# Performance work log

Hardware: AMD Instinct MI355X
Metric: run time of the kernel (lower is better)

Reference implementation:

```python
import jax, jax.numpy as jnp
import numpy as np

B, IN_F, OUT_F, K = 8192, 1024, 4096, 2
S = 64  # sqrt(OUT_F)


def setup_inputs() -> dict:
    key = jax.random.key(0)
    k1, k2, k3, k4 = jax.random.split(key, 4)
    x = jax.random.normal(k1, (B, IN_F), dtype=jnp.float32)
    y = jax.random.normal(k2, (B, OUT_F), dtype=jnp.float32)
    weight = jax.random.normal(k3, (OUT_F, IN_F), dtype=jnp.float32) * (1.0 / np.sqrt(IN_F))
    bias = jax.random.normal(k4, (OUT_F,), dtype=jnp.float32) * (1.0 / np.sqrt(IN_F))
    return {"x": x, "y": y, "weight": weight, "bias": bias}


def reference(x, y, weight, bias):
    # fused GEMM + bias + residual add epilogue
    out_lin = jnp.einsum('bk,nk->bn', x, weight) + bias + y  # (B, OUT_F)
    feat = out_lin.reshape(B, S, S)
    # AvgPool2d(kernel=K, stride=K)
    s_out = S // K
    pooled = feat.reshape(B, s_out, K, s_out, K).mean(axis=(2, 4))  # (B, s_out, s_out)
    # divide by global mean of the pooled map
    mean_val = pooled.mean()
    normed = pooled / mean_val
    return normed[:, None, :, :]  # (B, 1, s_out, s_out)
```

## Files before the change

### kernel.cpp

```cpp
#include <hip/hip_runtime.h>
#include <stdint.h>


#define KDIM 1024
#define NP   1024
#define BM 128
#define BN 128
#define BK 64

typedef __bf16 bf16x8 __attribute__((ext_vector_type(8)));
typedef float f32x4 __attribute__((ext_vector_type(4)));
typedef _Float16 f16x4 __attribute__((ext_vector_type(4)));

__device__ __forceinline__ unsigned f2bf(float f) {
  union { float f; unsigned u; } v; v.f = f;
  unsigned r = v.u + 0x7fffu + ((v.u >> 16) & 1u);
  return r >> 16;
}

__device__ __forceinline__ void gload_lds16(const void* g, void* l) {
  __builtin_amdgcn_global_load_lds(
      (const __attribute__((address_space(1))) void*)g,
      (__attribute__((address_space(3))) void*)l, 16, 0, 0);
}

__global__ void k_prep(const float* __restrict__ x, const float* __restrict__ W,
                       const float* __restrict__ bias,
                       unsigned short* __restrict__ xb, unsigned short* __restrict__ wp,
                       float* __restrict__ biasp) {
  int b = blockIdx.x;
  int t = threadIdx.x;
  if (b < 4096) {
    int i = b * 256 + t;
    const float4* x4 = (const float4*)x;
    float4 a = x4[i * 2], c = x4[i * 2 + 1];
    uint4 o;
    o.x = f2bf(a.x) | (f2bf(a.y) << 16);
    o.y = f2bf(a.z) | (f2bf(a.w) << 16);
    o.z = f2bf(c.x) | (f2bf(c.y) << 16);
    o.w = f2bf(c.z) | (f2bf(c.w) << 16);
    ((uint4*)xb)[i] = o;
  } else {
    int o = b - 4096;
    int r0 = ((o >> 5) << 7) + ((o & 31) << 1);
    const float4* W4 = (const float4*)W;
    float4 w0 = W4[(r0) * 256 + t];
    float4 w1 = W4[(r0 + 1) * 256 + t];
    float4 w2 = W4[(r0 + 64) * 256 + t];
    float4 w3 = W4[(r0 + 65) * 256 + t];
    float ax = 0.25f * (w0.x + w1.x + w2.x + w3.x);
    float ay = 0.25f * (w0.y + w1.y + w2.y + w3.y);
    float az = 0.25f * (w0.z + w1.z + w2.z + w3.z);
    float aw = 0.25f * (w0.w + w1.w + w2.w + w3.w);
    uint2 pk;
    pk.x = f2bf(ax) | (f2bf(ay) << 16);
    pk.y = f2bf(az) | (f2bf(aw) << 16);
    ((uint2*)wp)[o * 256 + t] = pk;
    if (t == 0)
      biasp[o] = 0.25f * (bias[r0] + bias[r0 + 1] + bias[r0 + 64] + bias[r0 + 65]);
  }
}

__global__ __launch_bounds__(512, 4) void k_gemm(
    const unsigned short* __restrict__ xb, const unsigned short* __restrict__ wp,
    const float* __restrict__ biasp, const float* __restrict__ y,
    float* __restrict__ out, _Float16* __restrict__ ph,
    float* __restrict__ partials, int use16) {
  __shared__ char smem[65536];

  int bid = blockIdx.x;
  int wg = (bid & 7) * 64 + (bid >> 3);
  int bm0 = (wg >> 3) * BM;
  int bn0 = (wg & 7) * BN;

  int tid = threadIdx.x;
  int lane = tid & 63;
  int wid = tid >> 6;
  int wr = wid >> 1, wc = wid & 1;

  f32x4 acc[2][4];
#pragma unroll
  for (int i = 0; i < 2; i++)
#pragma unroll
    for (int j = 0; j < 4; j++) acc[i][j] = (f32x4)0.0f;

  int srow = tid >> 3;
  int scol = (((lane & 7) ^ (lane >> 3)) << 3);
  const unsigned short* aSrc = xb + (size_t)(bm0 + srow) * KDIM + scol;
  const unsigned short* bSrc = wp + (size_t)(bn0 + srow) * KDIM + scol;
  int ldsOff = wid * 1024;

  int rbase = (lane & 15) * 128;
  int xorv = (lane & 7) << 4;
  int cb0 = (((lane >> 4) * 16)) ^ xorv;
  int cb1 = ((64 + (lane >> 4) * 16)) ^ xorv;

  const float2* y2 = (const float2*)y;
  int r_l = (lane >> 4) * 4;
  int c_l = lane & 15;
  int yrow0 = bm0 + wr * 32 + r_l;
  int yb[4];
#pragma unroll
  for (int ni = 0; ni < 4; ++ni) {
    int col = bn0 + wc * 64 + ni * 16 + c_l;
    yb[ni] = ((col >> 5) << 6) + (col & 31);
  }
  float2 yin[3][4];

#define STAGE(buf, ks)                                                         \
  {                                                                            \
    int k0 = (ks) * BK;                                                        \
    char* ab = smem + (buf) * 32768 + ldsOff;                                  \
    char* bb = smem + (buf) * 32768 + 16384 + ldsOff;                          \
    _Pragma("unroll")                                                          \
    for (int i = 0; i < 2; ++i)                                                \
      gload_lds16(aSrc + (size_t)i * 64 * KDIM + k0, ab + i * 8192);           \
    _Pragma("unroll")                                                          \
    for (int i = 0; i < 2; ++i)                                                \
      gload_lds16(bSrc + (size_t)i * 64 * KDIM + k0, bb + i * 8192);           \
  }

#define YLD(p, s, q)                                                           \
  {                                                                            \
    const float2* pp = y2 +                                                    \
        (size_t)(yrow0 + (((q) >> 4) * 16) + ((q) & 3)) * 2048 +               \
        yb[((q) >> 2) & 3];                                                    \
    asm volatile("global_load_dwordx2 %0, %1, off"                             \
                 : "=v"(yin[(p) % 3][s]) : "v"(pp) : "memory");                \
    asm volatile("global_load_dwordx2 %0, %1, off offset:256"                  \
                 : "=v"(yin[(p) % 3][(s) + 1]) : "v"(pp) : "memory");          \
  }
#define YLOAD(p) { YLD(p, 0, 2 * (p)) YLD(p, 2, 2 * (p) + 1) }
#define YCONS(p)                                                               \
  {                                                                            \
    acc[(2 * (p)) >> 4][((2 * (p)) >> 2) & 3][(2 * (p)) & 3] +=                \
        0.25f * ((yin[(p) % 3][0].x + yin[(p) % 3][0].y) +                     \
                 (yin[(p) % 3][1].x + yin[(p) % 3][1].y));                     \
    acc[(2 * (p) + 1) >> 4][((2 * (p) + 1) >> 2) & 3][(2 * (p) + 1) & 3] +=    \
        0.25f * ((yin[(p) % 3][2].x + yin[(p) % 3][2].y) +                     \
                 (yin[(p) % 3][3].x + yin[(p) % 3][3].y));                     \
  }

#define COMPUTE(cur)                                                           \
  {                                                                            \
    const char* Ab = smem + (cur) * 32768;                                     \
    const char* Bb = Ab + 16384;                                               \
    _Pragma("unroll")                                                          \
    for (int kk = 0; kk < 2; ++kk) {                                           \
      int cb = kk ? cb1 : cb0;                                                 \
      bf16x8 af[2], bfr[4];                                                    \
      _Pragma("unroll")                                                        \
      for (int mi = 0; mi < 2; ++mi)                                           \
        af[mi] = *(const bf16x8*)(Ab + (wr * 32 + mi * 16) * 128 + rbase + cb);\
      _Pragma("unroll")                                                        \
      for (int ni = 0; ni < 4; ++ni)                                           \
        bfr[ni] = *(const bf16x8*)(Bb + (wc * 64 + ni * 16) * 128 + rbase + cb);\
      _Pragma("unroll")                                                        \
      for (int mi = 0; mi < 2; ++mi)                                           \
        _Pragma("unroll")                                                      \
        for (int ni = 0; ni < 4; ++ni)                                         \
          acc[mi][ni] = __builtin_amdgcn_mfma_f32_16x16x32_bf16(               \
              af[mi], bfr[ni], acc[mi][ni], 0, 0, 0);                          \
    }                                                                          \
  }

#define KITER(ks, WAITSTR)                                                     \
  {                                                                            \
    if ((ks) < 15) STAGE(((ks) + 1) & 1, (ks) + 1);                            \
    YLOAD(ks);                                                                 \
    asm volatile(WAITSTR ::: "memory");                                        \
    __builtin_amdgcn_s_barrier();                                              \
    COMPUTE((ks) & 1);                                                         \
    __builtin_amdgcn_sched_barrier(0);                                         \
    if ((ks) >= 2) YCONS(((ks) >= 2 ? (ks) - 2 : 0));                          \
    asm volatile("" ::: "memory");                                             \
    __builtin_amdgcn_s_barrier();                                              \
  }

  STAGE(0, 0);
  KITER(0,  "s_waitcnt vmcnt(8)")
  KITER(1,  "s_waitcnt vmcnt(12)")
  KITER(2,  "s_waitcnt vmcnt(12)")
  KITER(3,  "s_waitcnt vmcnt(12)")
  KITER(4,  "s_waitcnt vmcnt(12)")
  KITER(5,  "s_waitcnt vmcnt(12)")
  KITER(6,  "s_waitcnt vmcnt(12)")
  KITER(7,  "s_waitcnt vmcnt(12)")
  KITER(8,  "s_waitcnt vmcnt(12)")
  KITER(9,  "s_waitcnt vmcnt(12)")
  KITER(10, "s_waitcnt vmcnt(12)")
  KITER(11, "s_waitcnt vmcnt(12)")
  KITER(12, "s_waitcnt vmcnt(12)")
  KITER(13, "s_waitcnt vmcnt(12)")
  KITER(14, "s_waitcnt vmcnt(12)")
  KITER(15, "s_waitcnt vmcnt(0)")
  __builtin_amdgcn_sched_barrier(0);
  YCONS(14);
  YCONS(15);

  float tsum = 0.f;
  float bpv[4];
#pragma unroll
  for (int ni = 0; ni < 4; ++ni) bpv[ni] = biasp[bn0 + wc * 64 + ni * 16 + c_l];
#pragma unroll
  for (int mi = 0; mi < 2; ++mi) {
#pragma unroll
    for (int ni = 0; ni < 4; ++ni) {
      int col = bn0 + wc * 64 + ni * 16 + c_l;
#pragma unroll
      for (int j = 0; j < 4; ++j) {
        int row = bm0 + wr * 32 + mi * 16 + r_l + j;
        float val = acc[mi][ni][j] + bpv[ni];
        size_t o = (size_t)row * NP + col;
        if (use16) ph[o] = (_Float16)val;
        else out[o] = val;
        tsum += val;
      }
    }
  }
#pragma unroll
  for (int off = 32; off > 0; off >>= 1) tsum += __shfl_down(tsum, off);
  float* sm = (float*)smem;
  __syncthreads();
  if (lane == 0) sm[wid] = tsum;
  __syncthreads();
  if (tid == 0)
    partials[bid] = ((sm[0] + sm[1]) + (sm[2] + sm[3])) +
                    ((sm[4] + sm[5]) + (sm[6] + sm[7]));
}

__global__ void k_norm(float* __restrict__ out, const _Float16* __restrict__ ph,
                       const float* __restrict__ partials, int use16) {
  __shared__ float s[256];
  int t = threadIdx.x;
  s[t] = partials[t] + partials[t + 256];
  __syncthreads();
#pragma unroll
  for (int off = 128; off > 0; off >>= 1) {
    if (t < off) s[t] += s[t + off];
    __syncthreads();
  }
  float inv = 8388608.0f / s[0];
  int i = blockIdx.x * 256 + t;
  float4* o4 = (float4*)out;
  if (use16) {
    f16x4 hv = ((const f16x4*)ph)[i];
    float4 v;
    v.x = (float)hv[0] * inv;
    v.y = (float)hv[1] * inv;
    v.z = (float)hv[2] * inv;
    v.w = (float)hv[3] * inv;
    o4[i] = v;
  } else {
    float4 v = o4[i];
    v.x *= inv; v.y *= inv; v.z *= inv; v.w *= inv;
    o4[i] = v;
  }
}

extern "C" void kernel_launch(void* const* d_in, const int* in_sizes, int n_in,
                              void* d_out, int out_size, void* d_ws, size_t ws_size,
                              hipStream_t stream) {
  (void)in_sizes; (void)n_in; (void)out_size;
  const float* x = (const float*)d_in[0];
  const float* y = (const float*)d_in[1];
  const float* W = (const float*)d_in[2];
  const float* bias = (const float*)d_in[3];
  float* out = (float*)d_out;

  char* ws = (char*)d_ws;
  unsigned short* xb = (unsigned short*)(ws);
  unsigned short* wp = (unsigned short*)(ws + 16777216);
  float* biasp = (float*)(ws + 16777216 + 2097152);
  float* partials = (float*)(ws + 16777216 + 2097152 + 4096);
  _Float16* ph = (_Float16*)(ws + 20971520);
  int use16 = (ws_size >= (size_t)20971520 + 16777216) ? 1 : 0;

  hipLaunchKernelGGL(k_prep, dim3(5120), dim3(256), 0, stream, x, W, bias, xb, wp, biasp);
  hipLaunchKernelGGL(k_gemm, dim3(512), dim3(512), 0, stream, xb, wp, biasp, y, out, ph, partials, use16);
  hipLaunchKernelGGL(k_norm, dim3(8192), dim3(256), 0, stream, out, ph, partials, use16);
}
```

Measured before the change: 57.84 us.

## Fuse x fp32-to-bf16 conversion into GEMM A-tile loading

Drops the separate x-to-bf16 pass in the prep kernel. The GEMM now loads fp32 x tiles into registers, converts them with v_cvt_pk_bf16_f32, and writes them to swizzled LDS after compute, while the B operand still uses direct global-to-LDS loads. This removes a 32MB read plus 16MB write round trip. In exchange it adds register pressure and VALU/LDS-store work in the main loop, and reduces the y prefetch depth from 3 stages to 2.

```diff
diff --git a/kernel.cpp b/kernel.cpp
--- a/kernel.cpp
+++ b/kernel.cpp
@@ -24,45 +24,30 @@
       (__attribute__((address_space(3))) void*)l, 16, 0, 0);
 }
 
-__global__ void k_prep(const float* __restrict__ x, const float* __restrict__ W,
-                       const float* __restrict__ bias,
-                       unsigned short* __restrict__ xb, unsigned short* __restrict__ wp,
-                       float* __restrict__ biasp) {
-  int b = blockIdx.x;
+__global__ void k_prep(const float* __restrict__ W, const float* __restrict__ bias,
+                       unsigned short* __restrict__ wp, float* __restrict__ biasp) {
+  int o = blockIdx.x;
   int t = threadIdx.x;
-  if (b < 4096) {
-    int i = b * 256 + t;
-    const float4* x4 = (const float4*)x;
-    float4 a = x4[i * 2], c = x4[i * 2 + 1];
-    uint4 o;
-    o.x = f2bf(a.x) | (f2bf(a.y) << 16);
-    o.y = f2bf(a.z) | (f2bf(a.w) << 16);
-    o.z = f2bf(c.x) | (f2bf(c.y) << 16);
-    o.w = f2bf(c.z) | (f2bf(c.w) << 16);
-    ((uint4*)xb)[i] = o;
-  } else {
-    int o = b - 4096;
-    int r0 = ((o >> 5) << 7) + ((o & 31) << 1);
-    const float4* W4 = (const float4*)W;
-    float4 w0 = W4[(r0) * 256 + t];
-    float4 w1 = W4[(r0 + 1) * 256 + t];
-    float4 w2 = W4[(r0 + 64) * 256 + t];
-    float4 w3 = W4[(r0 + 65) * 256 + t];
-    float ax = 0.25f * (w0.x + w1.x + w2.x + w3.x);
-    float ay = 0.25f * (w0.y + w1.y + w2.y + w3.y);
-    float az = 0.25f * (w0.z + w1.z + w2.z + w3.z);
-    float aw = 0.25f * (w0.w + w1.w + w2.w + w3.w);
-    uint2 pk;
-    pk.x = f2bf(ax) | (f2bf(ay) << 16);
-    pk.y = f2bf(az) | (f2bf(aw) << 16);
-    ((uint2*)wp)[o * 256 + t] = pk;
-    if (t == 0)
-      biasp[o] = 0.25f * (bias[r0] + bias[r0 + 1] + bias[r0 + 64] + bias[r0 + 65]);
-  }
+  int r0 = ((o >> 5) << 7) + ((o & 31) << 1);
+  const float4* W4 = (const float4*)W;
+  float4 w0 = W4[(r0) * 256 + t];
+  float4 w1 = W4[(r0 + 1) * 256 + t];
+  float4 w2 = W4[(r0 + 64) * 256 + t];
+  float4 w3 = W4[(r0 + 65) * 256 + t];
+  float ax = 0.25f * (w0.x + w1.x + w2.x + w3.x);
+  float ay = 0.25f * (w0.y + w1.y + w2.y + w3.y);
+  float az = 0.25f * (w0.z + w1.z + w2.z + w3.z);
+  float aw = 0.25f * (w0.w + w1.w + w2.w + w3.w);
+  uint2 pk;
+  pk.x = f2bf(ax) | (f2bf(ay) << 16);
+  pk.y = f2bf(az) | (f2bf(aw) << 16);
+  ((uint2*)wp)[o * 256 + t] = pk;
+  if (t == 0)
+    biasp[o] = 0.25f * (bias[r0] + bias[r0 + 1] + bias[r0 + 64] + bias[r0 + 65]);
 }
 
 __global__ __launch_bounds__(512, 4) void k_gemm(
-    const unsigned short* __restrict__ xb, const unsigned short* __restrict__ wp,
+    const float* __restrict__ x, const unsigned short* __restrict__ wp,
     const float* __restrict__ biasp, const float* __restrict__ y,
     float* __restrict__ out, _Float16* __restrict__ ph,
     float* __restrict__ partials, int use16) {
@@ -84,9 +69,14 @@
 #pragma unroll
     for (int j = 0; j < 4; j++) acc[i][j] = (f32x4)0.0f;
 
+  int arow = tid >> 2;
+  int aseg = tid & 3;
+  const float* aBase = x + (size_t)(bm0 + arow) * KDIM + aseg * 16;
+  int awAddr0 = arow * 128 + (((aseg * 2) ^ (arow & 7)) << 4);
+  int awAddr1 = arow * 128 + (((aseg * 2 + 1) ^ (arow & 7)) << 4);
+
   int srow = tid >> 3;
   int scol = (((lane & 7) ^ (lane >> 3)) << 3);
-  const unsigned short* aSrc = xb + (size_t)(bm0 + srow) * KDIM + scol;
   const unsigned short* bSrc = wp + (size_t)(bn0 + srow) * KDIM + scol;
   int ldsOff = wid * 1024;
 
@@ -105,19 +95,43 @@
     int col = bn0 + wc * 64 + ni * 16 + c_l;
     yb[ni] = ((col >> 5) << 6) + (col & 31);
   }
-  float2 yin[3][4];
-
-#define STAGE(buf, ks)                                                         \
+  float2 yin[2][4];
+  float4 a_in[4];
+
+#define ALOAD(ks)                                                              \
+  {                                                                            \
+    const float* ap = aBase + (ks) * BK;                                       \
+    asm volatile("global_load_dwordx4 %0, %1, off"                             \
+                 : "=v"(a_in[0]) : "v"(ap) : "memory");                        \
+    asm volatile("global_load_dwordx4 %0, %1, off offset:16"                   \
+                 : "=v"(a_in[1]) : "v"(ap) : "memory");                        \
+    asm volatile("global_load_dwordx4 %0, %1, off offset:32"                   \
+                 : "=v"(a_in[2]) : "v"(ap) : "memory");                        \
+    asm volatile("global_load_dwordx4 %0, %1, off offset:48"                   \
+                 : "=v"(a_in[3]) : "v"(ap) : "memory");                        \
+  }
+
+#define ACVT_WRITE(buf)                                                        \
+  {                                                                            \
+    uint4 w0, w1;                                                              \
+    asm("v_cvt_pk_bf16_f32 %0, %1, %2" : "=v"(w0.x) : "v"(a_in[0].x), "v"(a_in[0].y)); \
+    asm("v_cvt_pk_bf16_f32 %0, %1, %2" : "=v"(w0.y) : "v"(a_in[0].z), "v"(a_in[0].w)); \
+    asm("v_cvt_pk_bf16_f32 %0, %1, %2" : "=v"(w0.z) : "v"(a_in[1].x), "v"(a_in[1].y)); \
+    asm("v_cvt_pk_bf16_f32 %0, %1, %2" : "=v"(w0.w) : "v"(a_in[1].z), "v"(a_in[1].w)); \
+    asm("v_cvt_pk_bf16_f32 %0, %1, %2" : "=v"(w1.x) : "v"(a_in[2].x), "v"(a_in[2].y)); \
+    asm("v_cvt_pk_bf16_f32 %0, %1, %2" : "=v"(w1.y) : "v"(a_in[2].z), "v"(a_in[2].w)); \
+    asm("v_cvt_pk_bf16_f32 %0, %1, %2" : "=v"(w1.z) : "v"(a_in[3].x), "v"(a_in[3].y)); \
+    asm("v_cvt_pk_bf16_f32 %0, %1, %2" : "=v"(w1.w) : "v"(a_in[3].z), "v"(a_in[3].w)); \
+    *(uint4*)(smem + (buf) * 32768 + awAddr0) = w0;                            \
+    *(uint4*)(smem + (buf) * 32768 + awAddr1) = w1;                            \
+  }
+
+#define BSTAGE(buf, ks)                                                        \
   {                                                                            \
     int k0 = (ks) * BK;                                                        \
-    char* ab = smem + (buf) * 32768 + ldsOff;                                  \
     char* bb = smem + (buf) * 32768 + 16384 + ldsOff;                          \
-    _Pragma("unroll")                                                          \
-    for (int i = 0; i < 2; ++i)                                                \
-      gload_lds16(aSrc + (size_t)i * 64 * KDIM + k0, ab + i * 8192);           \
-    _Pragma("unroll")                                                          \
-    for (int i = 0; i < 2; ++i)                                                \
-      gload_lds16(bSrc + (size_t)i * 64 * KDIM + k0, bb + i * 8192);           \
+    gload_lds16(bSrc + (size_t)0 * 64 * KDIM + k0, bb + 0 * 8192);             \
+    gload_lds16(bSrc + (size_t)1 * 64 * KDIM + k0, bb + 1 * 8192);             \
   }
 
 #define YLD(p, s, q)                                                           \
@@ -126,19 +140,19 @@
         (size_t)(yrow0 + (((q) >> 4) * 16) + ((q) & 3)) * 2048 +               \
         yb[((q) >> 2) & 3];                                                    \
     asm volatile("global_load_dwordx2 %0, %1, off"                             \
-                 : "=v"(yin[(p) % 3][s]) : "v"(pp) : "memory");                \
+                 : "=v"(yin[(p) % 2][s]) : "v"(pp) : "memory");                \
     asm volatile("global_load_dwordx2 %0, %1, off offset:256"                  \
-                 : "=v"(yin[(p) % 3][(s) + 1]) : "v"(pp) : "memory");          \
+                 : "=v"(yin[(p) % 2][(s) + 1]) : "v"(pp) : "memory");          \
   }
 #define YLOAD(p) { YLD(p, 0, 2 * (p)) YLD(p, 2, 2 * (p) + 1) }
 #define YCONS(p)                                                               \
   {                                                                            \
     acc[(2 * (p)) >> 4][((2 * (p)) >> 2) & 3][(2 * (p)) & 3] +=                \
-        0.25f * ((yin[(p) % 3][0].x + yin[(p) % 3][0].y) +                     \
-                 (yin[(p) % 3][1].x + yin[(p) % 3][1].y));                     \
+        0.25f * ((yin[(p) % 2][0].x + yin[(p) % 2][0].y) +                     \
+                 (yin[(p) % 2][1].x + yin[(p) % 2][1].y));                     \
     acc[(2 * (p) + 1) >> 4][((2 * (p) + 1) >> 2) & 3][(2 * (p) + 1) & 3] +=    \
-        0.25f * ((yin[(p) % 3][2].x + yin[(p) % 3][2].y) +                     \
-                 (yin[(p) % 3][3].x + yin[(p) % 3][3].y));                     \
+        0.25f * ((yin[(p) % 2][2].x + yin[(p) % 2][2].y) +                     \
+                 (yin[(p) % 2][3].x + yin[(p) % 2][3].y));                     \
   }
 
 #define COMPUTE(cur)                                                           \
@@ -164,38 +178,49 @@
     }                                                                          \
   }
 
-#define KITER(ks, WAITSTR)                                                     \
-  {                                                                            \
-    if ((ks) < 15) STAGE(((ks) + 1) & 1, (ks) + 1);                            \
+#define KITER(ks, OPENWAIT)                                                    \
+  {                                                                            \
+    if ((ks) < 15) { ALOAD((ks) + 1); BSTAGE(((ks) + 1) & 1, (ks) + 1); }      \
     YLOAD(ks);                                                                 \
-    asm volatile(WAITSTR ::: "memory");                                        \
+    asm volatile(OPENWAIT ::: "memory");                                       \
     __builtin_amdgcn_s_barrier();                                              \
     COMPUTE((ks) & 1);                                                         \
     __builtin_amdgcn_sched_barrier(0);                                         \
-    if ((ks) >= 2) YCONS(((ks) >= 2 ? (ks) - 2 : 0));                          \
-    asm volatile("" ::: "memory");                                             \
+    if ((ks) < 15) {                                                           \
+      asm volatile("s_waitcnt vmcnt(6)" ::: "memory");                         \
+      __builtin_amdgcn_sched_barrier(0);                                       \
+      ACVT_WRITE(((ks) + 1) & 1);                                              \
+    }                                                                          \
+    if ((ks) >= 1) YCONS((ks) - 1);                                            \
+    asm volatile("s_waitcnt lgkmcnt(0)" ::: "memory");                         \
     __builtin_amdgcn_s_barrier();                                              \
   }
 
-  STAGE(0, 0);
-  KITER(0,  "s_waitcnt vmcnt(8)")
-  KITER(1,  "s_waitcnt vmcnt(12)")
-  KITER(2,  "s_waitcnt vmcnt(12)")
-  KITER(3,  "s_waitcnt vmcnt(12)")
-  KITER(4,  "s_waitcnt vmcnt(12)")
-  KITER(5,  "s_waitcnt vmcnt(12)")
-  KITER(6,  "s_waitcnt vmcnt(12)")
-  KITER(7,  "s_waitcnt vmcnt(12)")
-  KITER(8,  "s_waitcnt vmcnt(12)")
-  KITER(9,  "s_waitcnt vmcnt(12)")
-  KITER(10, "s_waitcnt vmcnt(12)")
-  KITER(11, "s_waitcnt vmcnt(12)")
-  KITER(12, "s_waitcnt vmcnt(12)")
-  KITER(13, "s_waitcnt vmcnt(12)")
-  KITER(14, "s_waitcnt vmcnt(12)")
-  KITER(15, "s_waitcnt vmcnt(0)")
+  ALOAD(0);
+  asm volatile("s_waitcnt vmcnt(0)" ::: "memory");
   __builtin_amdgcn_sched_barrier(0);
-  YCONS(14);
+  ACVT_WRITE(0);
+  BSTAGE(0, 0);
+
+  KITER(0,  "s_waitcnt vmcnt(10) lgkmcnt(0)")
+  KITER(1,  "s_waitcnt vmcnt(10)")
+  KITER(2,  "s_waitcnt vmcnt(10)")
+  KITER(3,  "s_waitcnt vmcnt(10)")
+  KITER(4,  "s_waitcnt vmcnt(10)")
+  KITER(5,  "s_waitcnt vmcnt(10)")
+  KITER(6,  "s_waitcnt vmcnt(10)")
+  KITER(7,  "s_waitcnt vmcnt(10)")
+  KITER(8,  "s_waitcnt vmcnt(10)")
+  KITER(9,  "s_waitcnt vmcnt(10)")
+  KITER(10, "s_waitcnt vmcnt(10)")
+  KITER(11, "s_waitcnt vmcnt(10)")
+  KITER(12, "s_waitcnt vmcnt(10)")
+  KITER(13, "s_waitcnt vmcnt(10)")
+  KITER(14, "s_waitcnt vmcnt(10)")
+  KITER(15, "s_waitcnt vmcnt(4)")
+
+  asm volatile("s_waitcnt vmcnt(0)" ::: "memory");
+  __builtin_amdgcn_sched_barrier(0);
   YCONS(15);
 
   float tsum = 0.f;
@@ -269,14 +294,13 @@
   float* out = (float*)d_out;
 
   char* ws = (char*)d_ws;
-  unsigned short* xb = (unsigned short*)(ws);
-  unsigned short* wp = (unsigned short*)(ws + 16777216);
-  float* biasp = (float*)(ws + 16777216 + 2097152);
-  float* partials = (float*)(ws + 16777216 + 2097152 + 4096);
-  _Float16* ph = (_Float16*)(ws + 20971520);
-  int use16 = (ws_size >= (size_t)20971520 + 16777216) ? 1 : 0;
-
-  hipLaunchKernelGGL(k_prep, dim3(5120), dim3(256), 0, stream, x, W, bias, xb, wp, biasp);
-  hipLaunchKernelGGL(k_gemm, dim3(512), dim3(512), 0, stream, xb, wp, biasp, y, out, ph, partials, use16);
+  unsigned short* wp = (unsigned short*)(ws);
+  float* biasp = (float*)(ws + 2097152);
+  float* partials = (float*)(ws + 2097152 + 4096);
+  _Float16* ph = (_Float16*)(ws + 4194304);
+  int use16 = (ws_size >= (size_t)4194304 + 16777216) ? 1 : 0;
+
+  hipLaunchKernelGGL(k_prep, dim3(1024), dim3(256), 0, stream, W, bias, wp, biasp);
+  hipLaunchKernelGGL(k_gemm, dim3(512), dim3(512), 0, stream, x, wp, biasp, y, out, ph, partials, use16);
   hipLaunchKernelGGL(k_norm, dim3(8192), dim3(256), 0, stream, out, ph, partials, use16);
 }
```

Result: slower. 69.29 us (+19.8%).
